# Performance work log

Measured on AMD Instinct MI355X. Metric: run time of the kernel, lower is better.

## Reference

```python
import jax, jax.numpy as jnp
import numpy as np

# model constants (ModelArgs defaults, 7B config)
H, D, BS = 32, 128, 8          # heads, head_dim, sparse_block_size
DIM = H * D                     # 4096
SINK_TOK, WIN_TOK, HEAVY = 60, 60, 1160
MB = HEAVY // BS                # 145 top blocks
T_CTX = 16384                   # prefilled context length


def apply_rope(x, freqs):
    # x: [B,S,H,D], freqs: [S, D//2, 2] -> rotate pairs as in apply_rotary_emb
    B, S, Hh, Dd = x.shape
    xs = x.reshape(B, S, Hh, Dd // 2, 2)
    fc = freqs.reshape(1, S, 1, Dd // 2, 2)
    xr, xi = xs[..., 0], xs[..., 1]
    fr, fi = fc[..., 0], fc[..., 1]
    out = jnp.stack([xr * fr - xi * fi, xi * fr + xr * fi], axis=-1)
    return out.reshape(B, S, Hh, Dd)


def setup_inputs() -> dict:
    key = jax.random.key(0)
    ks = jax.random.split(key, 6)
    B = 1
    return {
        'x': jax.random.normal(ks[0], (B, 1, DIM), jnp.float32),
        'freqs_cis': jax.random.normal(ks[1], (1, D // 2, 2), jnp.float32),
        'wqkv': jax.random.normal(ks[2], (3 * DIM, DIM), jnp.float32) * 0.02,
        'wo': jax.random.normal(ks[3], (DIM, DIM), jnp.float32) * 0.02,
        'k_cache': jax.random.normal(ks[4], (B, H, T_CTX, D), jnp.float32),
        'v_cache': jax.random.normal(ks[5], (B, H, T_CTX, D), jnp.float32),
        'input_pos': T_CTX - 1,
    }


def reference(x, freqs_cis, wqkv, wo, k_cache, v_cache, input_pos):
    B, S, _ = x.shape  # decode step, S == 1
    qkv = x @ wqkv.T                                   # [B,S,3*DIM]
    q, k, v = jnp.split(qkv, [DIM, 2 * DIM], axis=-1)
    q = q.reshape(B, S, H, D)
    k = k.reshape(B, S, H, D)
    v = v.reshape(B, S, H, D)
    q = apply_rope(q, freqs_cis)
    k = apply_rope(k, freqs_cis)

    # KV cache update at input_pos (token layout [B,H,T,D])
    k_bhsd = k.transpose(0, 2, 1, 3)
    v_bhsd = v.transpose(0, 2, 1, 3)
    kc = jax.lax.dynamic_update_slice(k_cache, k_bhsd, (0, 0, input_pos, 0))
    vc = jax.lax.dynamic_update_slice(v_cache, v_bhsd, (0, 0, input_pos, 0))

    T = input_pos + 1            # python int -> static
    Tb = T // BS                 # full blocks (T divisible by BS here)
    scale = 1.0 / np.sqrt(D).astype(np.float32)

    # block representative keys (k_sum_blk / k_cnt_blk mean) and routing scores
    k_mean = kc[:, :, :T].reshape(B, H, Tb, BS, D).mean(axis=3)   # [B,H,Tb,D]
    q1 = q[:, -1]                                                 # [B,H,D]
    scores = jnp.einsum('bhd,bhtd->bht', q1, k_mean) * scale      # [B,H,Tb]

    # build_block_index: sink + window + topk-Mb (static sizes)
    sink_b = min(-(-min(SINK_TOK, T) // BS), Tb)
    window_b = min(-(-min(WIN_TOK, T) // BS), Tb)
    cur_block = (T - 1) // BS
    win_start = max(0, cur_block - window_b + 1)
    win_end = cur_block + 1
    NEG = jnp.float32(-1e30)
    tb = jnp.arange(Tb)
    excl = (tb < sink_b) | ((tb >= win_start) & (tb < win_end))
    _, top_ids = jax.lax.top_k(jnp.where(excl, NEG, scores), MB)  # [B,H,MB]
    sink_ids = jnp.broadcast_to(jnp.arange(sink_b, dtype=jnp.int32), (B, H, sink_b))
    win_ids = jnp.broadcast_to(jnp.arange(win_start, win_end, dtype=jnp.int32), (B, H, win_end - win_start))
    block_index = jnp.concatenate([sink_ids, win_ids, top_ids.astype(jnp.int32)], axis=-1)  # [B,H,KLIST]

    # gather selected blocks' tokens and run restricted attention
    tok = (block_index[..., None] * BS + jnp.arange(BS, dtype=jnp.int32)).reshape(B, H, -1)  # [B,H,N]
    N = tok.shape[-1]
    valid = tok <= input_pos
    tok_c = jnp.clip(tok, 0, T - 1).astype(jnp.int32)
    idx = jnp.broadcast_to(tok_c[..., None], (B, H, N, D))
    k_sel = jnp.take_along_axis(kc, idx, axis=2)                  # [B,H,N,D]
    v_sel = jnp.take_along_axis(vc, idx, axis=2)
    att = jnp.einsum('bhd,bhnd->bhn', q1, k_sel) * scale
    p = jax.nn.softmax(jnp.where(valid, att, NEG), axis=-1)
    out = jnp.einsum('bhn,bhnd->bhd', p, v_sel)                   # [B,H,D]
    y = out.reshape(B, 1, DIM) @ wo.T                             # [B,1,DIM]
    return y
```

## Files before the change

### kernel.cpp

```cpp
#include <hip/hip_runtime.h>
#include <hip/hip_bf16.h>

#define NH 32
#define DH 128
#define DIMM 4096
#define TCTX 16384
#define BSZ 8
#define NBLK_TOT (TCTX / BSZ)
#define MB_SEL 145
#define SINK_TOK 60
#define WIN_TOK 60
#define BLK_CAP 192
#define NSPLIT 8
#define PSTRIDE (DH + 2)

__global__ __launch_bounds__(256) void k_gemv_qkv(const float* __restrict__ x,
                                                  const float* __restrict__ w,
                                                  const float* __restrict__ freqs,
                                                  float* __restrict__ q1,
                                                  float* __restrict__ kn,
                                                  float* __restrict__ vn) {
    __shared__ float xs[DIMM];
    __shared__ float acc4[4];
    int t = threadIdx.x;
    for (int i = t; i < DIMM / 4; i += 256)
        ((float4*)xs)[i] = ((const float4*)x)[i];
    __syncthreads();
    int wave = t >> 6, lane = t & 63;
    int row = blockIdx.x * 4 + wave;
    const float* wr = w + (size_t)row * DIMM;
    float acc = 0.f;
    #pragma unroll
    for (int it = 0; it < 16; ++it) {
        int j = lane * 4 + it * 256;
        float4 wv = *(const float4*)(wr + j);
        float4 xv = *(const float4*)(xs + j);
        acc += wv.x * xv.x + wv.y * xv.y + wv.z * xv.z + wv.w * xv.w;
    }
    #pragma unroll
    for (int m = 1; m < 64; m <<= 1) acc += __shfl_xor(acc, m, 64);
    if (lane == 0) acc4[wave] = acc;
    __syncthreads();
    if (t < 4) {
        int r = blockIdx.x * 4 + t;
        float a = acc4[t];
        if (r < 2 * DIMM) {
            float b = acc4[t ^ 1];
            int m = (r >> 1) & 63;
            float fr = freqs[2 * m], fi = freqs[2 * m + 1];
            float o = ((r & 1) == 0) ? (a * fr - b * fi) : (a * fr + b * fi);
            if (r < DIMM) q1[r] = o; else kn[r - DIMM] = o;
        } else {
            vn[r - 2 * DIMM] = a;
        }
    }
}

__global__ __launch_bounds__(256) void k_gemv_o(const float* __restrict__ x,
                                                const float* __restrict__ w,
                                                float* __restrict__ out) {
    __shared__ float xs[DIMM];
    int t = threadIdx.x;
    for (int i = t; i < DIMM / 4; i += 256)
        ((float4*)xs)[i] = ((const float4*)x)[i];
    __syncthreads();
    int wave = t >> 6, lane = t & 63;
    int row = blockIdx.x * 4 + wave;
    const float* wr = w + (size_t)row * DIMM;
    float acc = 0.f;
    #pragma unroll
    for (int it = 0; it < 16; ++it) {
        int j = lane * 4 + it * 256;
        float4 wv = *(const float4*)(wr + j);
        float4 xv = *(const float4*)(xs + j);
        acc += wv.x * xv.x + wv.y * xv.y + wv.z * xv.z + wv.w * xv.w;
    }
    #pragma unroll
    for (int m = 1; m < 64; m <<= 1) acc += __shfl_xor(acc, m, 64);
    if (lane == 0) out[row] = acc;
}

__global__ __launch_bounds__(256) void k_scores(const float* __restrict__ q1,
                                                const float* __restrict__ kc,
                                                const int* __restrict__ ip_p,
                                                float* __restrict__ scores) {
    int ip = *ip_p;
    int T = ip + 1;
    int Tb = T / BSZ;
    int wave = threadIdx.x >> 6, lane = threadIdx.x & 63;
    int h = blockIdx.x >> 9;
    int blk = ((blockIdx.x & 511) << 2) + wave;
    if (blk >= Tb) {
        if (blk < NBLK_TOT && lane == 0) scores[h * NBLK_TOT + blk] = -1e30f;
        return;
    }
    int d0 = (lane * 4) & 127;
    float4 q4 = *(const float4*)(q1 + h * DH + d0);
    const float* kb = kc + ((size_t)h * TCTX + (size_t)blk * BSZ) * DH;
    float acc = 0.f;
    #pragma unroll
    for (int i = 0; i < 4; ++i) {
        float4 k4 = *(const float4*)(kb + lane * 4 + i * 256);
        acc += q4.x * k4.x + q4.y * k4.y + q4.z * k4.z + q4.w * k4.w;
    }
    #pragma unroll
    for (int m = 1; m < 64; m <<= 1) acc += __shfl_xor(acc, m, 64);
    if (lane == 0) scores[h * NBLK_TOT + blk] = acc * 0.011048543456039805f;
}

__global__ __launch_bounds__(64) void k_topk(const float* __restrict__ scores,
                                             const int* __restrict__ ip_p,
                                             int* __restrict__ blklist) {
    int h = blockIdx.x;
    int lane = threadIdx.x & 63;
    int ip = *ip_p;
    int T = ip + 1;
    int Tb = T / BSZ;
    int sink_b = min((min(SINK_TOK, T) + BSZ - 1) / BSZ, Tb);
    int window_b = min((min(WIN_TOK, T) + BSZ - 1) / BSZ, Tb);
    int cur = (T - 1) / BSZ;
    int win_start = max(0, cur - window_b + 1);
    int win_end = cur + 1;

    unsigned int u[32];
    const float* sh = scores + h * NBLK_TOT;
    #pragma unroll
    for (int i = 0; i < 32; i += 4) {
        float4 sv = *(const float4*)(sh + lane * 32 + i);
        float fv[4] = {sv.x, sv.y, sv.z, sv.w};
        #pragma unroll
        for (int q = 0; q < 4; ++q) {
            int j = lane * 32 + i + q;
            unsigned int b = __float_as_uint(fv[q]);
            unsigned int m = (b & 0x80000000u) ? ~b : (b | 0x80000000u);
            bool ok = (j < Tb) && (j >= sink_b) && !(j >= win_start && j < win_end);
            u[i + q] = ok ? m : 0u;
        }
    }

    unsigned int lo = 0u, hi = 0xFFFFFFFFu;
    while (lo < hi) {
        unsigned int mid =
            (unsigned int)(((unsigned long long)lo + (unsigned long long)hi + 1ull) >> 1);
        int c = 0;
        #pragma unroll
        for (int i = 0; i < 32; ++i) c += (u[i] >= mid);
        #pragma unroll
        for (int m = 1; m < 64; m <<= 1) c += __shfl_xor(c, m, 64);
        if (c >= MB_SEL) lo = mid; else hi = mid - 1;
    }

    int gt = 0, eq = 0;
    #pragma unroll
    for (int i = 0; i < 32; ++i) { gt += (u[i] > lo); eq += (u[i] == lo); }
    unsigned int packed = ((unsigned int)gt << 16) | (unsigned int)eq;
    unsigned int sc = packed;
    #pragma unroll
    for (int off = 1; off < 64; off <<= 1) {
        unsigned int v = __shfl_up(sc, off, 64);
        if (lane >= off) sc += v;
    }
    unsigned int tot = __shfl(sc, 63, 64);
    unsigned int totg = tot >> 16;
    unsigned int excl = sc - packed;
    int gi = (int)(excl >> 16);
    int ei = (int)(excl & 0xFFFFu);
    int need_eq = MB_SEL - (int)totg;

    int base = sink_b + (win_end - win_start);
    int* bl = blklist + h * BLK_CAP;
    for (int i = lane; i < base; i += 64)
        bl[i] = (i < sink_b) ? i : (win_start + (i - sink_b));

    #pragma unroll
    for (int i = 0; i < 32; ++i) {
        int j = lane * 32 + i;
        if (u[i] > lo) {
            bl[base + gi] = j; ++gi;
        } else if (u[i] == lo) {
            if (ei < need_eq) bl[base + (int)totg + ei] = j;
            ++ei;
        }
    }
}

__global__ __launch_bounds__(256) void k_attn_part(const float* __restrict__ q1,
                                                   const float* __restrict__ kc,
                                                   const float* __restrict__ vc,
                                                   const float* __restrict__ kn,
                                                   const float* __restrict__ vn,
                                                   const int* __restrict__ blklist,
                                                   const int* __restrict__ ip_p,
                                                   float* __restrict__ part) {
    __shared__ float att[176];
    __shared__ float oacc[4][DH];
    __shared__ float redm[4];
    __shared__ int bl_s[24];
    int h = blockIdx.x / NSPLIT;
    int sp = blockIdx.x % NSPLIT;
    int t = threadIdx.x, wave = t >> 6, lane = t & 63;
    int g = lane >> 4, sub = lane & 15;
    int ip = *ip_p;
    int T = ip + 1;
    int Tb = T / BSZ;
    int sink_b = min((min(SINK_TOK, T) + BSZ - 1) / BSZ, Tb);
    int window_b = min((min(WIN_TOK, T) + BSZ - 1) / BSZ, Tb);
    int cur = (T - 1) / BSZ;
    int win_start = max(0, cur - window_b + 1);
    int nwin = cur + 1 - win_start;
    int nblk = sink_b + nwin + MB_SEL;
    int chunk = (nblk + NSPLIT - 1) / NSPLIT;
    int b0 = sp * chunk;
    int nb = min(nblk - b0, chunk);
    if (nb <= 0) nb = 0;
    int Ns = nb * BSZ;

    if (t < nb) bl_s[t] = blklist[h * BLK_CAP + b0 + t];
    __syncthreads();

    float4 qa = *(const float4*)(q1 + h * DH + sub * 8);
    float4 qb = *(const float4*)(q1 + h * DH + sub * 8 + 4);
    const float* kh = kc + (size_t)h * TCTX * DH;
    const float* vh = vc + (size_t)h * TCTX * DH;

    for (int c = wave; c < nb * 2; c += 4) {
        int blk = bl_s[c >> 1];
        int tok = blk * BSZ + (c & 1) * 4 + g;
        const float* kr = (tok == ip) ? (kn + h * DH) : (kh + (size_t)tok * DH);
        float4 ka = *(const float4*)(kr + sub * 8);
        float4 kb2 = *(const float4*)(kr + sub * 8 + 4);
        float p = qa.x * ka.x + qa.y * ka.y + qa.z * ka.z + qa.w * ka.w +
                  qb.x * kb2.x + qb.y * kb2.y + qb.z * kb2.z + qb.w * kb2.w;
        p += __shfl_xor(p, 1, 64);
        p += __shfl_xor(p, 2, 64);
        p += __shfl_xor(p, 4, 64);
        p += __shfl_xor(p, 8, 64);
        if (sub == 0) att[c * 4 + g] = p * 0.08838834764831845f;
    }
    __syncthreads();

    float mx = -1e30f;
    for (int n = t; n < Ns; n += 256) mx = fmaxf(mx, att[n]);
    #pragma unroll
    for (int m = 1; m < 64; m <<= 1) mx = fmaxf(mx, __shfl_xor(mx, m, 64));
    if (lane == 0) redm[wave] = mx;
    __syncthreads();
    mx = fmaxf(fmaxf(redm[0], redm[1]), fmaxf(redm[2], redm[3]));
    __syncthreads();
    float sum = 0.f;
    for (int n = t; n < Ns; n += 256) {
        float e = __expf(att[n] - mx);
        att[n] = e;
        sum += e;
    }
    #pragma unroll
    for (int m = 1; m < 64; m <<= 1) sum += __shfl_xor(sum, m, 64);
    if (lane == 0) redm[wave] = sum;
    __syncthreads();
    float lsum = redm[0] + redm[1] + redm[2] + redm[3];

    float4 aa = make_float4(0, 0, 0, 0), ab = make_float4(0, 0, 0, 0);
    for (int c = wave; c < nb * 2; c += 4) {
        int blk = bl_s[c >> 1];
        int tok = blk * BSZ + (c & 1) * 4 + g;
        const float* vr = (tok == ip) ? (vn + h * DH) : (vh + (size_t)tok * DH);
        float p = att[c * 4 + g];
        float4 va = *(const float4*)(vr + sub * 8);
        float4 vb = *(const float4*)(vr + sub * 8 + 4);
        aa.x += p * va.x; aa.y += p * va.y; aa.z += p * va.z; aa.w += p * va.w;
        ab.x += p * vb.x; ab.y += p * vb.y; ab.z += p * vb.z; ab.w += p * vb.w;
    }
    #pragma unroll
    for (int m = 16; m < 64; m <<= 1) {
        aa.x += __shfl_xor(aa.x, m, 64); aa.y += __shfl_xor(aa.y, m, 64);
        aa.z += __shfl_xor(aa.z, m, 64); aa.w += __shfl_xor(aa.w, m, 64);
        ab.x += __shfl_xor(ab.x, m, 64); ab.y += __shfl_xor(ab.y, m, 64);
        ab.z += __shfl_xor(ab.z, m, 64); ab.w += __shfl_xor(ab.w, m, 64);
    }
    if (g == 0) {
        oacc[wave][sub * 8 + 0] = aa.x; oacc[wave][sub * 8 + 1] = aa.y;
        oacc[wave][sub * 8 + 2] = aa.z; oacc[wave][sub * 8 + 3] = aa.w;
        oacc[wave][sub * 8 + 4] = ab.x; oacc[wave][sub * 8 + 5] = ab.y;
        oacc[wave][sub * 8 + 6] = ab.z; oacc[wave][sub * 8 + 7] = ab.w;
    }
    __syncthreads();
    float* pp = part + ((size_t)h * NSPLIT + sp) * PSTRIDE;
    if (t < DH)
        pp[t] = oacc[0][t] + oacc[1][t] + oacc[2][t] + oacc[3][t];
    if (t == DH)     pp[DH] = mx;
    if (t == DH + 1) pp[DH + 1] = lsum;
}

__global__ __launch_bounds__(128) void k_attn_reduce(const float* __restrict__ part,
                                                     float* __restrict__ o) {
    int h = blockIdx.x, t = threadIdx.x;
    const float* ph = part + (size_t)h * NSPLIT * PSTRIDE;
    float M = -1e30f;
    float ml[NSPLIT];
    float ll[NSPLIT];
    #pragma unroll
    for (int s = 0; s < NSPLIT; ++s) {
        ml[s] = ph[s * PSTRIDE + DH];
        ll[s] = ph[s * PSTRIDE + DH + 1];
        M = fmaxf(M, ml[s]);
    }
    float L = 0.f, acc = 0.f;
    #pragma unroll
    for (int s = 0; s < NSPLIT; ++s) {
        float w = __expf(ml[s] - M);
        L += ll[s] * w;
        acc += ph[s * PSTRIDE + t] * w;
    }
    o[h * DH + t] = acc / L;
}

extern "C" void kernel_launch(void* const* d_in, const int* in_sizes, int n_in,
                              void* d_out, int out_size, void* d_ws, size_t ws_size,
                              hipStream_t stream) {
    const float* x     = (const float*)d_in[0];
    const float* freqs = (const float*)d_in[1];
    const float* wqkv  = (const float*)d_in[2];
    const float* wo    = (const float*)d_in[3];
    const float* kc    = (const float*)d_in[4];
    const float* vc    = (const float*)d_in[5];
    const int*   ip    = (const int*)d_in[6];
    float* y = (float*)d_out;

    float* ws     = (float*)d_ws;
    float* q1     = ws;
    float* kn     = ws + 4096;
    float* vn     = ws + 8192;
    float* scores = ws + 12288;
    float* part   = ws + 77824;
    float* o      = ws + 111104;
    int*   blkl   = (int*)(ws + 115200);

    k_gemv_qkv<<<3 * DIMM / 4, 256, 0, stream>>>(x, wqkv, freqs, q1, kn, vn);
    k_scores<<<NH * 512, 256, 0, stream>>>(q1, kc, ip, scores);
    k_topk<<<NH, 64, 0, stream>>>(scores, ip, blkl);
    k_attn_part<<<NH * NSPLIT, 256, 0, stream>>>(q1, kc, vc, kn, vn, blkl, ip, part);
    k_attn_reduce<<<NH, 128, 0, stream>>>(part, o);
    k_gemv_o<<<DIMM / 4, 256, 0, stream>>>(o, wo, y);
}
```

Baseline: 135.6 us.

## Raise attention split count to 32 and compute two block scores per wave

```diff
diff --git a/kernel.cpp b/kernel.cpp
--- a/kernel.cpp
+++ b/kernel.cpp
@@ -11,7 +11,7 @@
 #define SINK_TOK 60
 #define WIN_TOK 60
 #define BLK_CAP 192
-#define NSPLIT 8
+#define NSPLIT 32
 #define PSTRIDE (DH + 2)
 
 __global__ __launch_bounds__(256) void k_gemv_qkv(const float* __restrict__ x,
@@ -88,24 +88,38 @@
     int T = ip + 1;
     int Tb = T / BSZ;
     int wave = threadIdx.x >> 6, lane = threadIdx.x & 63;
-    int h = blockIdx.x >> 9;
-    int blk = ((blockIdx.x & 511) << 2) + wave;
-    if (blk >= Tb) {
-        if (blk < NBLK_TOT && lane == 0) scores[h * NBLK_TOT + blk] = -1e30f;
-        return;
-    }
+    int h = blockIdx.x >> 8;
+    int blk0 = (((blockIdx.x & 255) << 2) + wave) * 2;
     int d0 = (lane * 4) & 127;
     float4 q4 = *(const float4*)(q1 + h * DH + d0);
-    const float* kb = kc + ((size_t)h * TCTX + (size_t)blk * BSZ) * DH;
-    float acc = 0.f;
-    #pragma unroll
-    for (int i = 0; i < 4; ++i) {
-        float4 k4 = *(const float4*)(kb + lane * 4 + i * 256);
-        acc += q4.x * k4.x + q4.y * k4.y + q4.z * k4.z + q4.w * k4.w;
-    }
-    #pragma unroll
-    for (int m = 1; m < 64; m <<= 1) acc += __shfl_xor(acc, m, 64);
-    if (lane == 0) scores[h * NBLK_TOT + blk] = acc * 0.011048543456039805f;
+    float a0 = 0.f, a1 = 0.f;
+    if (blk0 < Tb) {
+        const float* kb = kc + ((size_t)h * TCTX + (size_t)blk0 * BSZ) * DH;
+        #pragma unroll
+        for (int i = 0; i < 4; ++i) {
+            float4 k4 = *(const float4*)(kb + lane * 4 + i * 256);
+            a0 += q4.x * k4.x + q4.y * k4.y + q4.z * k4.z + q4.w * k4.w;
+        }
+    }
+    if (blk0 + 1 < Tb) {
+        const float* kb = kc + ((size_t)h * TCTX + (size_t)(blk0 + 1) * BSZ) * DH;
+        #pragma unroll
+        for (int i = 0; i < 4; ++i) {
+            float4 k4 = *(const float4*)(kb + lane * 4 + i * 256);
+            a1 += q4.x * k4.x + q4.y * k4.y + q4.z * k4.z + q4.w * k4.w;
+        }
+    }
+    #pragma unroll
+    for (int m = 1; m < 64; m <<= 1) {
+        a0 += __shfl_xor(a0, m, 64);
+        a1 += __shfl_xor(a1, m, 64);
+    }
+    if (lane == 0) {
+        float2 out;
+        out.x = (blk0 < Tb) ? a0 * 0.011048543456039805f : -1e30f;
+        out.y = (blk0 + 1 < Tb) ? a1 * 0.011048543456039805f : -1e30f;
+        *(float2*)(scores + h * NBLK_TOT + blk0) = out;
+    }
 }
 
 __global__ __launch_bounds__(64) void k_topk(const float* __restrict__ scores,
@@ -192,10 +206,10 @@
                                                    const int* __restrict__ blklist,
                                                    const int* __restrict__ ip_p,
                                                    float* __restrict__ part) {
-    __shared__ float att[176];
+    __shared__ float att[48];
     __shared__ float oacc[4][DH];
     __shared__ float redm[4];
-    __shared__ int bl_s[24];
+    __shared__ int bl_s[8];
     int h = blockIdx.x / NSPLIT;
     int sp = blockIdx.x % NSPLIT;
     int t = threadIdx.x, wave = t >> 6, lane = t & 63;
@@ -212,7 +226,13 @@
     int chunk = (nblk + NSPLIT - 1) / NSPLIT;
     int b0 = sp * chunk;
     int nb = min(nblk - b0, chunk);
-    if (nb <= 0) nb = 0;
+    float* pp = part + ((size_t)h * NSPLIT + sp) * PSTRIDE;
+    if (nb <= 0) {
+        if (t < DH) pp[t] = 0.f;
+        if (t == DH) pp[DH] = -1e30f;
+        if (t == DH + 1) pp[DH + 1] = 0.f;
+        return;
+    }
     int Ns = nb * BSZ;
 
     if (t < nb) bl_s[t] = blklist[h * BLK_CAP + b0 + t];
@@ -284,7 +304,6 @@
         oacc[wave][sub * 8 + 6] = ab.z; oacc[wave][sub * 8 + 7] = ab.w;
     }
     __syncthreads();
-    float* pp = part + ((size_t)h * NSPLIT + sp) * PSTRIDE;
     if (t < DH)
         pp[t] = oacc[0][t] + oacc[1][t] + oacc[2][t] + oacc[3][t];
     if (t == DH)     pp[DH] = mx;
@@ -296,19 +315,13 @@
     int h = blockIdx.x, t = threadIdx.x;
     const float* ph = part + (size_t)h * NSPLIT * PSTRIDE;
     float M = -1e30f;
-    float ml[NSPLIT];
-    float ll[NSPLIT];
-    #pragma unroll
+    #pragma unroll 8
+    for (int s = 0; s < NSPLIT; ++s) M = fmaxf(M, ph[s * PSTRIDE + DH]);
+    float L = 0.f, acc = 0.f;
+    #pragma unroll 8
     for (int s = 0; s < NSPLIT; ++s) {
-        ml[s] = ph[s * PSTRIDE + DH];
-        ll[s] = ph[s * PSTRIDE + DH + 1];
-        M = fmaxf(M, ml[s]);
-    }
-    float L = 0.f, acc = 0.f;
-    #pragma unroll
-    for (int s = 0; s < NSPLIT; ++s) {
-        float w = __expf(ml[s] - M);
-        L += ll[s] * w;
+        float w = __expf(ph[s * PSTRIDE + DH] - M);
+        L += ph[s * PSTRIDE + DH + 1] * w;
         acc += ph[s * PSTRIDE + t] * w;
     }
     o[h * DH + t] = acc / L;
@@ -332,11 +345,11 @@
     float* vn     = ws + 8192;
     float* scores = ws + 12288;
     float* part   = ws + 77824;
-    float* o      = ws + 111104;
-    int*   blkl   = (int*)(ws + 115200);
+    float* o      = ws + 210944;
+    int*   blkl   = (int*)(ws + 215040);
 
     k_gemv_qkv<<<3 * DIMM / 4, 256, 0, stream>>>(x, wqkv, freqs, q1, kn, vn);
-    k_scores<<<NH * 512, 256, 0, stream>>>(q1, kc, ip, scores);
+    k_scores<<<NH * 256, 256, 0, stream>>>(q1, kc, ip, scores);
     k_topk<<<NH, 64, 0, stream>>>(scores, ip, blkl);
     k_attn_part<<<NH * NSPLIT, 256, 0, stream>>>(q1, kc, vc, kn, vn, blkl, ip, part);
     k_attn_reduce<<<NH, 128, 0, stream>>>(part, o);
```

New measurement: 137.5 us. No clear change (+1.4%).
